# Kernel tuning notes

Hardware: AMD Instinct MI355X
Metric: run time of the kernel (lower is better)

## Reference

```python
import jax, jax.numpy as jnp
import numpy as np

DIM = 192
HEADS = 4
HID = int(DIM * 2.66)  # 510, Restormer GDFN hidden dim
EPS_LN = 1e-6


def ln2d(x, w, b):
    # torch LayerNorm2d variant: global mean/std over (C,H,W), std is UNBIASED (ddof=1)
    n = x.shape[1] * x.shape[2] * x.shape[3]
    mean = x.mean(axis=(1, 2, 3), keepdims=True)
    var = ((x - mean) ** 2).sum(axis=(1, 2, 3), keepdims=True) / (n - 1)
    return (x - mean) / (jnp.sqrt(var) + EPS_LN) * w + b


def conv1x1(x, w):
    # w: [O, C]; pointwise conv as channel matmul
    return jnp.einsum('bchw,oc->bohw', x, w)


def dwconv3(x, w):
    # w: [C, 1, 3, 3] depthwise 3x3, padding=1
    return jax.lax.conv_general_dilated(
        x, w, window_strides=(1, 1), padding='SAME',
        dimension_numbers=('NCHW', 'OIHW', 'NCHW'),
        feature_group_count=x.shape[1])


def setup_inputs() -> dict:
    key = jax.random.key(0)
    ks = jax.random.split(key, 8)
    s = 0.02
    return {
        'x': jax.random.normal(ks[0], (2, DIM, 256, 256), dtype=jnp.float32),
        'n1_w': jnp.ones((1, DIM, 1, 1), jnp.float32),
        'n1_b': jnp.zeros((1, DIM, 1, 1), jnp.float32),
        'qkv_w': jax.random.normal(ks[1], (3 * DIM, DIM), jnp.float32) * s,
        'qkv_dw_w': jax.random.normal(ks[2], (3 * DIM, 1, 3, 3), jnp.float32) * s,
        'proj_w': jax.random.normal(ks[3], (DIM, DIM), jnp.float32) * s,
        'temperature': jnp.ones((HEADS, 1, 1), jnp.float32),
        'n2_w': jnp.ones((1, DIM, 1, 1), jnp.float32),
        'n2_b': jnp.zeros((1, DIM, 1, 1), jnp.float32),
        'ff_in_w': jax.random.normal(ks[4], (2 * HID, DIM), jnp.float32) * s,
        'ff_dw_w': jax.random.normal(ks[5], (2 * HID, 1, 3, 3), jnp.float32) * s,
        'ff_out_w': jax.random.normal(ks[6], (DIM, HID), jnp.float32) * s,
    }


def reference(x, n1_w, n1_b, qkv_w, qkv_dw_w, proj_w, temperature,
              n2_w, n2_b, ff_in_w, ff_dw_w, ff_out_w):
    b, c, h, w = x.shape
    hd = c // HEADS

    # ---- MDTA attention ----
    y = ln2d(x, n1_w, n1_b)
    qkv = dwconv3(conv1x1(y, qkv_w), qkv_dw_w)  # [b, 3c, h, w]
    q, k, v = jnp.split(qkv, 3, axis=1)
    q = q.reshape(b, HEADS, hd, h * w)
    k = k.reshape(b, HEADS, hd, h * w)
    v = v.reshape(b, HEADS, hd, h * w)
    # L2-normalize along spatial axis (F.normalize, eps=1e-12)
    q = q / jnp.maximum(jnp.linalg.norm(q, axis=-1, keepdims=True), 1e-12)
    k = k / jnp.maximum(jnp.linalg.norm(k, axis=-1, keepdims=True), 1e-12)
    attn = jnp.einsum('bhcn,bhdn->bhcd', q, k) * temperature  # [b,H,hd,hd]
    attn = jax.nn.softmax(attn, axis=-1)
    out = jnp.einsum('bhcd,bhdn->bhcn', attn, v).reshape(b, c, h, w)
    x = x + conv1x1(out, proj_w)

    # ---- GDFN feed-forward ----
    y = ln2d(x, n2_w, n2_b)
    y = dwconv3(conv1x1(y, ff_in_w), ff_dw_w)  # [b, 2*HID, h, w]
    x1, x2 = jnp.split(y, 2, axis=1)
    y = jax.nn.gelu(x1, approximate=False) * x2
    x = x + conv1x1(y, ff_out_w)
    return x
```

## Files before the change

### kernel.cpp

```cpp
#include <hip/hip_runtime.h>
#include <hip/hip_bf16.h>

typedef unsigned short u16;
typedef __attribute__((ext_vector_type(8))) short short8;
typedef __attribute__((ext_vector_type(8))) unsigned short ushort8v;
typedef __attribute__((ext_vector_type(4))) float f32x4;

#define NPIX  65536
#define HH    256
#define WW    256
#define BATCH 2
#define CDIM  192
#define NHEADS 4
#define HD    48
#define OQKV  576
#define HIDN  510
#define OPAD  1024

__device__ __forceinline__ float bf2f(u16 b) {
  union { unsigned u; float f; } v; v.u = ((unsigned)b) << 16; return v.f;
}
__device__ __forceinline__ u16 f2bf(float f) {
  union { float f; unsigned u; } v; v.f = f;
  unsigned r = v.u + 0x7fffu + ((v.u >> 16) & 1u);
  return (u16)(r >> 16);
}
__device__ __forceinline__ void atomAddF(float* p, float v) { unsafeAtomicAdd(p, v); }
__device__ __forceinline__ void gload16(const void* g, void* l) {
  __builtin_amdgcn_global_load_lds((const __attribute__((address_space(1))) unsigned int*)g,
                                   (__attribute__((address_space(3))) unsigned int*)l, 16, 0, 0);
}
__device__ __forceinline__ void xcdswz(int& bx, int& by) {
  const int nx = gridDim.x;
  const int tot = nx * gridDim.y;
  const int lin = by * nx + bx;
  const int q = tot >> 3, r = tot & 7;
  const int xcd = lin & 7, pos = lin >> 3;
  const int nl = (xcd < r) ? (xcd * (q + 1) + pos) : (r * (q + 1) + (xcd - r) * q + pos);
  bx = nl % nx; by = nl / nx;
}
__device__ __forceinline__ void dw3row(const u16* __restrict__ rp, int jm, bool hasL, bool hasR,
                                       float w0, float w1, float w2, float* acc) {
  ushort8v m = *(const ushort8v*)(rp + jm);
  float f[10];
  f[0] = hasL ? bf2f(rp[jm - 1]) : 0.f;
  #pragma unroll
  for (int t = 0; t < 8; ++t) f[t + 1] = bf2f(m[t]);
  f[9] = hasR ? bf2f(rp[jm + 8]) : 0.f;
  #pragma unroll
  for (int i = 0; i < 8; ++i) acc[i] += w0 * f[i] + w1 * f[i + 1] + w2 * f[i + 2];
}

#define OFF_STATS1 ((size_t)0)
#define OFF_STATS2 ((size_t)64)
#define OFF_G      ((size_t)128)
#define OFF_NQ     (OFF_G + 73728)
#define OFF_NK     (OFF_NQ + 1536)
#define ZERO_BYTES (OFF_NK + 1536)
#define OFF_BQ     ((size_t)77056)
#define OFF_B2     (OFF_BQ + 4608)
#define OFF_M      (OFF_B2 + 8192)
#define OFF_WQ     (OFF_M + 294912)
#define OFF_W2B    (OFF_WQ + 442368)
#define OFF_W3     (OFF_W2B + 786432)
#define OFF_T      (OFF_W3 + 196608)
#define OFF_QKV    (OFF_T + 50331648)
#define OFF_BAND   (OFF_QKV + 150994944)

__global__ __launch_bounds__(256) void k_statsT(const float* __restrict__ P, u16* __restrict__ T,
                                                float* __restrict__ stats) {
  __shared__ u16 ld[128][200];
  const int b = blockIdx.y, n0 = blockIdx.x * 128, tid = threadIdx.x;
  const float* Pb = P + (((size_t)b * CDIM) << 16) + n0;
  float s = 0.f, ss = 0.f;
  for (int it = 0; it < 24; ++it) {
    int idx = it * 256 + tid;
    int c = idx >> 5, j = idx & 31;
    float4 v = *(const float4*)(Pb + ((size_t)c << 16) + j * 4);
    s  += v.x + v.y + v.z + v.w;
    ss += v.x*v.x + v.y*v.y + v.z*v.z + v.w*v.w;
    int px = j * 4;
    ld[px][c] = f2bf(v.x); ld[px+1][c] = f2bf(v.y);
    ld[px+2][c] = f2bf(v.z); ld[px+3][c] = f2bf(v.w);
  }
  for (int off = 32; off; off >>= 1) { s += __shfl_down(s, off); ss += __shfl_down(ss, off); }
  __shared__ float ls[4], lss[4];
  const int wid = tid >> 6, lane = tid & 63;
  if (lane == 0) { ls[wid] = s; lss[wid] = ss; }
  __syncthreads();
  if (tid == 0) {
    atomAddF(&stats[b*2+0], ls[0]+ls[1]+ls[2]+ls[3]);
    atomAddF(&stats[b*2+1], lss[0]+lss[1]+lss[2]+lss[3]);
  }
  u16* Tb = T + (size_t)(b * NPIX + n0) * CDIM;
  for (int it = 0; it < 12; ++it) {
    int idx = it * 256 + tid;
    int ch = idx % 24, nl = idx / 24;
    union { u16 s[8]; uint4 v; } t;
    #pragma unroll
    for (int r = 0; r < 8; ++r) t.s[r] = ld[nl][ch * 8 + r];
    int sch = ch ^ (nl & 7);
    *(uint4*)((char*)(Tb + (size_t)nl * CDIM) + sch * 16) = t.v;
  }
}

__global__ void k_fold(const float* __restrict__ w_in, const float* __restrict__ ln_w,
                       const float* __restrict__ ln_b, const float* __restrict__ stats,
                       u16* __restrict__ W, float* __restrict__ bias, int O_real) {
  const int o = blockIdx.x, b = blockIdx.y, c = threadIdx.x;
  const int Mtot = gridDim.x;
  const float n = (float)(CDIM * NPIX);
  const float sum = stats[b*2], sumsq = stats[b*2+1];
  const float mean = sum / n;
  const float var = (sumsq - sum * sum / n) / (n - 1.f);
  const float inv = 1.f / (sqrtf(var) + 1e-6f);
  float we = 0.f, cb = 0.f;
  if (o < O_real) {
    float wi = w_in[o * CDIM + c];
    float a  = ln_w[c] * inv;
    we = wi * a;
    cb = wi * (ln_b[c] - mean * a);
  }
  int sch = (c >> 3) ^ (o & 7);
  W[((size_t)b * Mtot + o) * CDIM + sch * 8 + (c & 7)] = f2bf(we);
  for (int off = 32; off; off >>= 1) cb += __shfl_down(cb, off);
  __shared__ float l[3];
  if ((threadIdx.x & 63) == 0) l[threadIdx.x >> 6] = cb;
  __syncthreads();
  if (threadIdx.x == 0) bias[b * Mtot + o] = l[0] + l[1] + l[2];
}

__global__ void k_fold3(const float* __restrict__ w, u16* __restrict__ W3) {
  const int o = blockIdx.x;
  for (int it = 0; it < 2; ++it) {
    int c = it * 256 + threadIdx.x;
    float v = (c < HIDN) ? w[o * HIDN + c] : 0.f;
    int sch = (c >> 3) ^ (o & 7);
    W3[o * 512 + sch * 8 + (c & 7)] = f2bf(v);
  }
}

template <int KTOT, int KC, int EPI, int STATS>
__global__ __launch_bounds__(256) void k_mgemm(
    const u16* __restrict__ Bm, const u16* __restrict__ Am,
    const float* __restrict__ bias,
    const u16* __restrict__ rT, long rTbstr,
    void* __restrict__ outv, long Obstr, int out_nstr,
    u16* __restrict__ tout, long toutbstr,
    int Mtot, long Bbstr, long Abstr,
    int nB_base, int nB_rows, int nO_base, float* __restrict__ stats)
{
  constexpr int RBC = KC * 2;
  __shared__ u16 lB[128 * KC];
  __shared__ u16 lA[64 * KC];
  const int b = blockIdx.z;
  int bx = blockIdx.x, by = blockIdx.y;
  xcdswz(bx, by);
  const int o0 = bx * 64;
  const int nB = nB_base + by * 128;
  const int nO = nO_base + by * 128;
  const int tid = threadIdx.x;
  const int lane = tid & 63;
  const int wid = tid >> 6;

  if (EPI == 0 && (nB < 0 || nB >= nB_rows)) {
    u16* op = (u16*)outv;
    uint4 z; z.x = z.y = z.z = z.w = 0u;
    for (int it = 0; it < 4; ++it) {
      int idx = it * 256 + tid;
      int orow = idx >> 4, c8 = idx & 15;
      *(uint4*)(op + (size_t)b * Obstr + (size_t)(o0 + orow) * out_nstr + nO + c8 * 8) = z;
    }
    return;
  }

  const u16* Bb = Bm + (size_t)b * Bbstr + (size_t)nB * KTOT;
  const u16* Ab = Am + (size_t)b * Abstr + (size_t)o0 * KTOT;

  f32x4 acc[4][2];
  #pragma unroll
  for (int m = 0; m < 4; ++m)
    #pragma unroll
    for (int nf = 0; nf < 2; ++nf) acc[m][nf] = (f32x4){0.f, 0.f, 0.f, 0.f};

  for (int kc0 = 0; kc0 < KTOT; kc0 += KC) {
    if (kc0) __syncthreads();
    if constexpr (KTOT == KC) {
      #pragma unroll
      for (int it = 0; it < 128 * RBC / 16 / 256; ++it) {
        int idx = it * 256 + tid;
        gload16((const char*)Bb + idx * 16, (char*)lB + idx * 16);
      }
      #pragma unroll
      for (int it = 0; it < 64 * RBC / 16 / 256; ++it) {
        int idx = it * 256 + tid;
        gload16((const char*)Ab + idx * 16, (char*)lA + idx * 16);
      }
    } else {
      constexpr int NCH = KC / 8;
      #pragma unroll
      for (int it = 0; it < 128 * NCH / 256; ++it) {
        int idx = it * 256 + tid; int r = idx / NCH, ch = idx % NCH;
        gload16((const char*)(Bb + (size_t)r * KTOT + kc0) + ch * 16, (char*)lB + idx * 16);
      }
      #pragma unroll
      for (int it = 0; it < 64 * NCH / 256; ++it) {
        int idx = it * 256 + tid; int r = idx / NCH, ch = idx % NCH;
        gload16((const char*)(Ab + (size_t)r * KTOT + kc0) + ch * 16, (char*)lA + idx * 16);
      }
    }
    __syncthreads();
    const int lr = lane & 15, g = lane >> 4;
    #pragma unroll
    for (int ks = 0; ks < KC / 32; ++ks) {
      const int ck = ks * 4 + g;
      short8 afr[4], bfr[2];
      #pragma unroll
      for (int m = 0; m < 4; ++m) {
        int row = m * 16 + lr;
        afr[m] = *(const short8*)((const char*)lA + row * RBC + ((ck ^ (row & 7)) << 4));
      }
      #pragma unroll
      for (int nf = 0; nf < 2; ++nf) {
        int row = wid * 32 + nf * 16 + lr;
        bfr[nf] = *(const short8*)((const char*)lB + row * RBC + ((ck ^ (row & 7)) << 4));
      }
      #pragma unroll
      for (int m = 0; m < 4; ++m)
        #pragma unroll
        for (int nf = 0; nf < 2; ++nf)
          acc[m][nf] = __builtin_amdgcn_mfma_f32_16x16x32_bf16(afr[m], bfr[nf], acc[m][nf], 0, 0, 0);
    }
  }

  const int col = lane & 15, rg = lane >> 4;
  if constexpr (EPI == 0) {
    u16* op = (u16*)outv;
    #pragma unroll
    for (int m = 0; m < 4; ++m)
      #pragma unroll
      for (int j = 0; j < 4; ++j) {
        int o = o0 + m * 16 + rg * 4 + j;
        float bv = bias[b * Mtot + o];
        #pragma unroll
        for (int nf = 0; nf < 2; ++nf) {
          int nn = nO + wid * 32 + nf * 16 + col;
          op[(size_t)b * Obstr + (size_t)o * out_nstr + nn] = f2bf(acc[m][nf][j] + bv);
        }
      }
  } else if constexpr (EPI == 2) {
    float* lBf = (float*)lB;
    __syncthreads();
    #pragma unroll
    for (int m = 0; m < 4; ++m)
      #pragma unroll
      for (int nf = 0; nf < 2; ++nf)
        #pragma unroll
        for (int j = 0; j < 4; ++j)
          lBf[(wid * 32 + nf * 16 + col) * 66 + m * 16 + rg * 4 + j] = acc[m][nf][j];
    __syncthreads();
    float s = 0.f, ss = 0.f;
    for (int it = 0; it < 4; ++it) {
      int idx = it * 256 + tid;
      int n = idx >> 3, ch3 = idx & 7;
      size_t rowoff = (size_t)(nO + n) * CDIM;
      int chunk = (o0 >> 3) + (ch3 ^ (n & 7));
      uint4 xv = *(const uint4*)((const char*)(rT + (size_t)b * rTbstr + rowoff) + chunk * 16);
      u16* xs = (u16*)&xv;
      union { u16 s[8]; uint4 v; } t;
      #pragma unroll
      for (int r = 0; r < 8; ++r) {
        float rv = bf2f(xs[r]) + lBf[n * 66 + ch3 * 8 + r];
        t.s[r] = f2bf(rv);
        if constexpr (STATS) { s += rv; ss += rv * rv; }
      }
      *(uint4*)((char*)(tout + (size_t)b * toutbstr + rowoff) + chunk * 16) = t.v;
    }
    if constexpr (STATS) {
      for (int off = 32; off; off >>= 1) { s += __shfl_down(s, off); ss += __shfl_down(ss, off); }
      __shared__ float sr1[4], sr2[4];
      if (lane == 0) { sr1[wid] = s; sr2[wid] = ss; }
      __syncthreads();
      if (tid == 0) {
        atomAddF(&stats[b*2+0], sr1[0]+sr1[1]+sr1[2]+sr1[3]);
        atomAddF(&stats[b*2+1], sr2[0]+sr2[1]+sr2[2]+sr2[3]);
      }
    }
  } else {
    u16* lAx = lA;
    __syncthreads();
    for (int it = 0; it < 4; ++it) {
      int idx = it * 256 + tid;
      int n = idx >> 3, ch3 = idx & 7;
      int chunk = (o0 >> 3) + (ch3 ^ (n & 7));
      uint4 xv = *(const uint4*)((const char*)(rT + (size_t)b * rTbstr + (size_t)(nO + n) * CDIM) + chunk * 16);
      u16* xs = (u16*)&xv;
      #pragma unroll
      for (int r = 0; r < 8; ++r) lAx[n * 66 + ch3 * 8 + r] = xs[r];
    }
    __syncthreads();
    float* of = (float*)outv;
    #pragma unroll
    for (int m = 0; m < 4; ++m)
      #pragma unroll
      for (int nf = 0; nf < 2; ++nf)
        #pragma unroll
        for (int j = 0; j < 4; ++j) {
          int o = o0 + m * 16 + rg * 4 + j;
          int nl = wid * 32 + nf * 16 + col;
          size_t ix = (size_t)b * Obstr + (size_t)o * out_nstr + nO + nl;
          of[ix] = acc[m][nf][j] + bf2f(lAx[nl * 66 + m * 16 + rg * 4 + j]);
        }
  }
}

__global__ __launch_bounds__(256) void k_gram(const u16* __restrict__ qkv,
                                              const float* __restrict__ dww,
                                              float* __restrict__ G,
                                              float* __restrict__ nq,
                                              float* __restrict__ nk) {
  __shared__ u16 qs[HD][264], ks2[HD][264];
  __shared__ u16 wq[HD][9], wk[HD][9];
  __shared__ float nql[HD], nkl[HD];
  int bx = blockIdx.x, by = blockIdx.y;
  xcdswz(bx, by);
  const int b = by >> 2, h = by & 3;
  const int row = bx;
  const int tid = threadIdx.x;

  for (int idx = tid; idx < HD * 9; idx += 256) {
    int c = idx / 9, k9 = idx % 9;
    wq[c][k9] = f2bf(dww[(h * HD + c) * 9 + k9]);
    wk[c][k9] = f2bf(dww[(CDIM + h * HD + c) * 9 + k9]);
  }
  if (tid < HD) { nql[tid] = 0.f; nkl[tid] = 0.f; }
  __syncthreads();

  for (int it = 0; it < 12; ++it) {
    int idx = it * 256 + tid;
    int j = idx & 31, cz = idx >> 5;
    int c = cz % HD, qk = cz / HD;
    const u16* base = qkv + (((size_t)(b * OQKV + qk * CDIM + h * HD + c)) << 16);
    const u16* w = qk ? wk[c] : wq[c];
    float acc[8] = {0.f,0.f,0.f,0.f,0.f,0.f,0.f,0.f};
    const int jm = j * 8;
    const bool hasL = j > 0, hasR = j < 31;
    if (row > 0)   dw3row(base + (row - 1) * 256, jm, hasL, hasR, bf2f(w[0]), bf2f(w[1]), bf2f(w[2]), acc);
                   dw3row(base + row * 256,       jm, hasL, hasR, bf2f(w[3]), bf2f(w[4]), bf2f(w[5]), acc);
    if (row < 255) dw3row(base + (row + 1) * 256, jm, hasL, hasR, bf2f(w[6]), bf2f(w[7]), bf2f(w[8]), acc);
    union { u16 s[8]; ushort8v v; } rv;
    float sqs = 0.f;
    #pragma unroll
    for (int i = 0; i < 8; ++i) {
      rv.s[i] = f2bf(acc[i]);
      float vv = bf2f(rv.s[i]);
      sqs += vv * vv;
    }
    if (qk) { *(ushort8v*)&ks2[c][jm] = rv.v; atomicAdd(&nkl[c], sqs); }
    else    { *(ushort8v*)&qs[c][jm]  = rv.v; atomicAdd(&nql[c], sqs); }
  }
  __syncthreads();

  if (tid < HD) atomAddF(&nq[(b*NHEADS+h)*HD + tid], nql[tid]);
  else if (tid < 2*HD) atomAddF(&nk[(b*NHEADS+h)*HD + tid - HD], nkl[tid - HD]);

  const int lane = tid & 63, wid = tid >> 6;
  const int lr = lane & 15, g = lane >> 4;
  float* Gb = G + (size_t)(b * NHEADS + h) * HD * HD;
  for (int t = wid; t < 9; t += 4) {
    const int m = t / 3, nb = t % 3;
    f32x4 a4 = (f32x4){0.f, 0.f, 0.f, 0.f};
    #pragma unroll
    for (int ksi = 0; ksi < 8; ++ksi) {
      int off = ksi * 32 + g * 8;
      short8 af = *(const short8*)&qs[m * 16 + lr][off];
      short8 bf = *(const short8*)&ks2[nb * 16 + lr][off];
      a4 = __builtin_amdgcn_mfma_f32_16x16x32_bf16(af, bf, a4, 0, 0, 0);
    }
    #pragma unroll
    for (int jj = 0; jj < 4; ++jj)
      atomAddF(&Gb[(m * 16 + g * 4 + jj) * HD + nb * 16 + lr], a4[jj]);
  }
}

__global__ void k_attnM(const float* __restrict__ G, const float* __restrict__ nq,
                        const float* __restrict__ nk, const float* __restrict__ temp,
                        const float* __restrict__ proj_w, u16* __restrict__ Mb16) {
  const int h = blockIdx.x, b = blockIdx.y;
  __shared__ float at[HD][HD];
  const float* Gb = G + (size_t)(b * NHEADS + h) * HD * HD;
  const float* nqb = nq + (b * NHEADS + h) * HD;
  const float* nkb = nk + (b * NHEADS + h) * HD;
  const float t = temp[h];
  const int tid = threadIdx.x;
  for (int idx = tid; idx < HD * HD; idx += 256) {
    int c = idx / HD, d = idx % HD;
    float qn = fmaxf(sqrtf(nqb[c]), 1e-12f);
    float kn = fmaxf(sqrtf(nkb[d]), 1e-12f);
    at[c][d] = Gb[idx] / (qn * kn) * t;
  }
  __syncthreads();
  if (tid < HD) {
    float m = -1e30f;
    for (int d = 0; d < HD; ++d) m = fmaxf(m, at[tid][d]);
    float s = 0.f;
    for (int d = 0; d < HD; ++d) { float e = __expf(at[tid][d] - m); at[tid][d] = e; s += e; }
    float inv = 1.f / s;
    for (int d = 0; d < HD; ++d) at[tid][d] *= inv;
  }
  __syncthreads();
  for (int idx = tid; idx < CDIM * HD; idx += 256) {
    int o = idx / HD, d = idx % HD;
    float acc = 0.f;
    for (int c = 0; c < HD; ++c) acc += proj_w[o * CDIM + h * HD + c] * at[c][d];
    int cf = h * HD + d;
    int sch = (cf >> 3) ^ (o & 7);
    Mb16[((size_t)(b * CDIM + o)) * CDIM + sch * 8 + (cf & 7)] = f2bf(acc);
  }
}

__global__ __launch_bounds__(256) void k_dwT(const u16* __restrict__ qkv,
                                             const float* __restrict__ dww,
                                             u16* __restrict__ vdwT, long vdwbstr) {
  __shared__ u16 ld[64][201];
  __shared__ float w9[CDIM][9];
  int bx = blockIdx.x, by = blockIdx.y;
  xcdswz(bx, by);
  const int b = by;
  const int p0 = bx * 64;
  const int row = p0 >> 8, col0 = p0 & 255;
  const int tid = threadIdx.x;
  for (int idx = tid; idx < CDIM * 9; idx += 256) w9[idx / 9][idx % 9] = dww[384 * 9 + idx];
  __syncthreads();
  for (int it = 0; it < 6; ++it) {
    int idx = it * 256 + tid;
    int j = idx & 7, c = idx >> 3;
    const u16* base = qkv + (((size_t)(b * OQKV + 384 + c)) << 16);
    const float* w = w9[c];
    float acc[8] = {0.f,0.f,0.f,0.f,0.f,0.f,0.f,0.f};
    const int jm = col0 + j * 8;
    const bool hasL = jm > 0, hasR = jm < 248;
    if (row > 0)   dw3row(base + (row - 1) * 256, jm, hasL, hasR, w[0], w[1], w[2], acc);
                   dw3row(base + row * 256,       jm, hasL, hasR, w[3], w[4], w[5], acc);
    if (row < 255) dw3row(base + (row + 1) * 256, jm, hasL, hasR, w[6], w[7], w[8], acc);
    #pragma unroll
    for (int i = 0; i < 8; ++i) ld[j * 8 + i][c] = f2bf(acc[i]);
  }
  __syncthreads();
  u16* Tb = vdwT + (size_t)b * vdwbstr + (size_t)p0 * CDIM;
  for (int it = 0; it < 6; ++it) {
    int idx = it * 256 + tid;
    int ch = idx % 24, pl = idx / 24;
    union { u16 s[8]; uint4 v; } t;
    #pragma unroll
    for (int r = 0; r < 8; ++r) t.s[r] = ld[pl][ch * 8 + r];
    int sch = ch ^ (pl & 7);
    *(uint4*)((char*)(Tb + (size_t)pl * CDIM) + sch * 16) = t.v;
  }
}

__global__ __launch_bounds__(256) void k_dwgT(const u16* __restrict__ hp_, const float* __restrict__ w9,
                                              u16* __restrict__ ygT, int rows_loc, int band_px) {
  __shared__ u16 ld[64][523];
  int bx = blockIdx.x, by = blockIdx.y;
  xcdswz(bx, by);
  const int b = by;
  const int p0 = bx * 64;
  const int olr = p0 >> 8, col0 = p0 & 255;
  const int tid = threadIdx.x;
  if (tid < 128) {
    int px = tid >> 1, c = 510 + (tid & 1);
    ld[px][c] = 0;
  }
  __syncthreads();
  for (int it = 0; it < 16; ++it) {
    int idx = it * 256 + tid;
    if (idx >= HIDN * 8) break;
    int j = idx & 7, c = idx >> 3;
    const u16* ia = hp_ + (size_t)(b * OPAD + c) * rows_loc * 256;
    const u16* ig = hp_ + (size_t)(b * OPAD + c + HIDN) * rows_loc * 256;
    float aa[8] = {0.f,0.f,0.f,0.f,0.f,0.f,0.f,0.f};
    float gg[8] = {0.f,0.f,0.f,0.f,0.f,0.f,0.f,0.f};
    const int jm = col0 + j * 8;
    const bool hasL = jm > 0, hasR = jm < 248;
    #pragma unroll
    for (int dr = 0; dr < 3; ++dr) {
      dw3row(ia + (olr + dr) * 256, jm, hasL, hasR,
             w9[c * 9 + dr * 3], w9[c * 9 + dr * 3 + 1], w9[c * 9 + dr * 3 + 2], aa);
      dw3row(ig + (olr + dr) * 256, jm, hasL, hasR,
             w9[(c + HIDN) * 9 + dr * 3], w9[(c + HIDN) * 9 + dr * 3 + 1],
             w9[(c + HIDN) * 9 + dr * 3 + 2], gg);
    }
    #pragma unroll
    for (int i = 0; i < 8; ++i) {
      float a = aa[i];
      float gel = 0.5f * a * (1.f + erff(a * 0.70710678118654752f));
      ld[j * 8 + i][c] = f2bf(gel * gg[i]);
    }
  }
  __syncthreads();
  u16* Tb = ygT + ((size_t)b * band_px + p0) * 512;
  for (int it = 0; it < 16; ++it) {
    int idx = it * 256 + tid;
    int ch = idx & 63, pl = idx >> 6;
    union { u16 s[8]; uint4 v; } t;
    #pragma unroll
    for (int r = 0; r < 8; ++r) t.s[r] = ld[pl][ch * 8 + r];
    int sch = ch ^ (pl & 7);
    *(uint4*)((char*)(Tb + (size_t)pl * 512) + sch * 16) = t.v;
  }
}

extern "C" void kernel_launch(void* const* d_in, const int* in_sizes, int n_in,
                              void* d_out, int out_size, void* d_ws, size_t ws_size,
                              hipStream_t stream) {
  const float* x       = (const float*)d_in[0];
  const float* n1_w    = (const float*)d_in[1];
  const float* n1_b    = (const float*)d_in[2];
  const float* qkv_w   = (const float*)d_in[3];
  const float* qkv_dw  = (const float*)d_in[4];
  const float* proj_w  = (const float*)d_in[5];
  const float* temp    = (const float*)d_in[6];
  const float* n2_w    = (const float*)d_in[7];
  const float* n2_b    = (const float*)d_in[8];
  const float* ff_in_w = (const float*)d_in[9];
  const float* ff_dw   = (const float*)d_in[10];
  const float* ff_out_w= (const float*)d_in[11];

  char* ws = (char*)d_ws;
  float* stats1 = (float*)(ws + OFF_STATS1);
  float* stats2 = (float*)(ws + OFF_STATS2);
  float* G      = (float*)(ws + OFF_G);
  float* nq     = (float*)(ws + OFF_NQ);
  float* nk     = (float*)(ws + OFF_NK);
  float* biasq  = (float*)(ws + OFF_BQ);
  float* bias2  = (float*)(ws + OFF_B2);
  u16*   Mb16   = (u16*)(ws + OFF_M);
  u16*   Wq     = (u16*)(ws + OFF_WQ);
  u16*   W2b    = (u16*)(ws + OFF_W2B);
  u16*   W3     = (u16*)(ws + OFF_W3);
  u16*   xT     = (u16*)(ws + OFF_T);
  u16*   qkv    = (u16*)(ws + OFF_QKV);
  u16*   vdwT   = qkv;
  u16*   x2T    = qkv + (size_t)CDIM * NPIX;
  const long qkvbstr = (long)OQKV * NPIX;
  float* outp   = (float*)d_out;

  int NP = 32;
  const int cand[4] = {2, 4, 8, 16};
  for (int i = 0; i < 4; ++i) {
    int rws = 256 / cand[i], rl = rws + 2;
    size_t band = (size_t)2 * OPAD * rl * 256 * 2 + (size_t)2 * rws * 256 * 512 * 2;
    if (OFF_BAND + band + ((size_t)8 << 20) <= ws_size) { NP = cand[i]; break; }
  }
  const int rows = 256 / NP, rows_loc = rows + 2, band_px = rows * 256;
  u16* hpre = (u16*)(ws + OFF_BAND);
  u16* ygT  = (u16*)(ws + OFF_BAND + (size_t)2 * OPAD * rows_loc * 256 * 2);

  hipMemsetAsync(ws, 0, ZERO_BYTES, stream);

  k_statsT<<<dim3(NPIX / 128, BATCH), 256, 0, stream>>>(x, xT, stats1);
  k_fold<<<dim3(OQKV, BATCH), CDIM, 0, stream>>>(qkv_w, n1_w, n1_b, stats1, Wq, biasq, OQKV);
  k_mgemm<192, 192, 0, 0><<<dim3(OQKV / 64, NPIX / 128, BATCH), 256, 0, stream>>>(
      xT, Wq, biasq, nullptr, 0L, qkv, (long)OQKV * NPIX, NPIX, nullptr, 0L,
      OQKV, (long)NPIX * CDIM, (long)OQKV * CDIM, 0, NPIX, 0, nullptr);
  k_gram<<<dim3(256, BATCH * NHEADS), 256, 0, stream>>>(qkv, qkv_dw, G, nq, nk);
  k_attnM<<<dim3(NHEADS, BATCH), 256, 0, stream>>>(G, nq, nk, temp, proj_w, Mb16);
  k_dwT<<<dim3(NPIX / 64, BATCH), 256, 0, stream>>>(qkv, qkv_dw, vdwT, qkvbstr);
  k_mgemm<192, 192, 2, 1><<<dim3(CDIM / 64, NPIX / 128, BATCH), 256, 0, stream>>>(
      vdwT, Mb16, nullptr, xT, (long)NPIX * CDIM, nullptr, 0L, 0, x2T, qkvbstr,
      CDIM, qkvbstr, (long)CDIM * CDIM, 0, NPIX, 0, stats2);

  k_fold<<<dim3(OPAD, BATCH), CDIM, 0, stream>>>(ff_in_w, n2_w, n2_b, stats2, W2b, bias2, 1020);
  k_fold3<<<dim3(CDIM), 256, 0, stream>>>(ff_out_w, W3);
  for (int rp = 0; rp < NP; ++rp) {
    const int band0 = rp * band_px;
    k_mgemm<192, 192, 0, 0><<<dim3(OPAD / 64, rows_loc * 2, BATCH), 256, 0, stream>>>(
        x2T, W2b, bias2, nullptr, 0L, hpre, (long)OPAD * rows_loc * 256, rows_loc * 256,
        nullptr, 0L, OPAD, qkvbstr, (long)OPAD * CDIM, band0 - 256, NPIX, 0, nullptr);
    k_dwgT<<<dim3(band_px / 64, BATCH), 256, 0, stream>>>(hpre, ff_dw, ygT, rows_loc, band_px);
    k_mgemm<512, 256, 3, 0><<<dim3(CDIM / 64, rows * 2, BATCH), 256, 0, stream>>>(
        ygT, W3, nullptr, x2T, qkvbstr, outp, (long)CDIM * NPIX, NPIX, nullptr, 0L,
        CDIM, (long)band_px * 512, 0L, 0, band_px, band0, nullptr);
  }
}
```

Baseline: 892.7 us.

## Spread reduction atomics over slots and shrink GEMM K-chunks for occupancy

Global atomic accumulators for LayerNorm statistics, the Gram matrix and the q/k norms are spread over 32 slots, so blocks stop contending on the same addresses. The consumers (fold, attnM) sum the slots when they read them. The GEMM kernels now use smaller K chunks (64 or 128 instead of 192 or 256) in a single union LDS buffer that the epilogue reuses, which cuts shared memory per block and should allow more resident blocks. The cost is extra K-loop iterations with more barriers, and a larger zeroed workspace. The swizzle must stay correct when K is chunked.

Result: faster. 807.7 us (-9.5%).

```diff
diff --git a/kernel.cpp b/kernel.cpp
--- a/kernel.cpp
+++ b/kernel.cpp
@@ -16,6 +16,7 @@
 #define OQKV  576
 #define HIDN  510
 #define OPAD  1024
+#define NSLOT 32
 
 __device__ __forceinline__ float bf2f(u16 b) {
   union { unsigned u; float f; } v; v.u = ((unsigned)b) << 16; return v.f;
@@ -52,12 +53,12 @@
 }
 
 #define OFF_STATS1 ((size_t)0)
-#define OFF_STATS2 ((size_t)64)
-#define OFF_G      ((size_t)128)
-#define OFF_NQ     (OFF_G + 73728)
-#define OFF_NK     (OFF_NQ + 1536)
-#define ZERO_BYTES (OFF_NK + 1536)
-#define OFF_BQ     ((size_t)77056)
+#define OFF_STATS2 ((size_t)512)
+#define OFF_G      ((size_t)1024)
+#define OFF_NQ     (OFF_G + 2359296)
+#define OFF_NK     (OFF_NQ + 49152)
+#define ZERO_BYTES (OFF_NK + 49152)
+#define OFF_BQ     ZERO_BYTES
 #define OFF_B2     (OFF_BQ + 4608)
 #define OFF_M      (OFF_B2 + 8192)
 #define OFF_WQ     (OFF_M + 294912)
@@ -71,6 +72,7 @@
                                                 float* __restrict__ stats) {
   __shared__ u16 ld[128][200];
   const int b = blockIdx.y, n0 = blockIdx.x * 128, tid = threadIdx.x;
+  const int slot = blockIdx.x & (NSLOT - 1);
   const float* Pb = P + (((size_t)b * CDIM) << 16) + n0;
   float s = 0.f, ss = 0.f;
   for (int it = 0; it < 24; ++it) {
@@ -89,8 +91,8 @@
   if (lane == 0) { ls[wid] = s; lss[wid] = ss; }
   __syncthreads();
   if (tid == 0) {
-    atomAddF(&stats[b*2+0], ls[0]+ls[1]+ls[2]+ls[3]);
-    atomAddF(&stats[b*2+1], lss[0]+lss[1]+lss[2]+lss[3]);
+    atomAddF(&stats[(slot * BATCH + b) * 2 + 0], ls[0]+ls[1]+ls[2]+ls[3]);
+    atomAddF(&stats[(slot * BATCH + b) * 2 + 1], lss[0]+lss[1]+lss[2]+lss[3]);
   }
   u16* Tb = T + (size_t)(b * NPIX + n0) * CDIM;
   for (int it = 0; it < 12; ++it) {
@@ -110,7 +112,11 @@
   const int o = blockIdx.x, b = blockIdx.y, c = threadIdx.x;
   const int Mtot = gridDim.x;
   const float n = (float)(CDIM * NPIX);
-  const float sum = stats[b*2], sumsq = stats[b*2+1];
+  float sum = 0.f, sumsq = 0.f;
+  for (int sl = 0; sl < NSLOT; ++sl) {
+    sum   += stats[(sl * BATCH + b) * 2 + 0];
+    sumsq += stats[(sl * BATCH + b) * 2 + 1];
+  }
   const float mean = sum / n;
   const float var = (sumsq - sum * sum / n) / (n - 1.f);
   const float inv = 1.f / (sqrtf(var) + 1e-6f);
@@ -151,8 +157,12 @@
     int nB_base, int nB_rows, int nO_base, float* __restrict__ stats)
 {
   constexpr int RBC = KC * 2;
-  __shared__ u16 lB[128 * KC];
-  __shared__ u16 lA[64 * KC];
+  constexpr int LDSB = (128 + 64) * KC * 2;
+  constexpr int EPIB = (EPI == 2) ? 128 * 66 * 4 : ((EPI == 3) ? 128 * 66 * 2 : 0);
+  constexpr int TOT  = LDSB > EPIB ? LDSB : EPIB;
+  __shared__ char lds[TOT];
+  u16* lB = (u16*)lds;
+  u16* lA = (u16*)(lds + 128 * KC * 2);
   const int b = blockIdx.z;
   int bx = blockIdx.x, by = blockIdx.y;
   xcdswz(bx, by);
@@ -185,29 +195,16 @@
 
   for (int kc0 = 0; kc0 < KTOT; kc0 += KC) {
     if (kc0) __syncthreads();
-    if constexpr (KTOT == KC) {
-      #pragma unroll
-      for (int it = 0; it < 128 * RBC / 16 / 256; ++it) {
-        int idx = it * 256 + tid;
-        gload16((const char*)Bb + idx * 16, (char*)lB + idx * 16);
-      }
-      #pragma unroll
-      for (int it = 0; it < 64 * RBC / 16 / 256; ++it) {
-        int idx = it * 256 + tid;
-        gload16((const char*)Ab + idx * 16, (char*)lA + idx * 16);
-      }
-    } else {
-      constexpr int NCH = KC / 8;
-      #pragma unroll
-      for (int it = 0; it < 128 * NCH / 256; ++it) {
-        int idx = it * 256 + tid; int r = idx / NCH, ch = idx % NCH;
-        gload16((const char*)(Bb + (size_t)r * KTOT + kc0) + ch * 16, (char*)lB + idx * 16);
-      }
-      #pragma unroll
-      for (int it = 0; it < 64 * NCH / 256; ++it) {
-        int idx = it * 256 + tid; int r = idx / NCH, ch = idx % NCH;
-        gload16((const char*)(Ab + (size_t)r * KTOT + kc0) + ch * 16, (char*)lA + idx * 16);
-      }
+    constexpr int NCH = KC / 8;
+    #pragma unroll
+    for (int it = 0; it < 128 * NCH / 256; ++it) {
+      int idx = it * 256 + tid; int r = idx / NCH, ch = idx % NCH;
+      gload16((const char*)(Bb + (size_t)r * KTOT + kc0) + ch * 16, (char*)lB + idx * 16);
+    }
+    #pragma unroll
+    for (int it = 0; it < 64 * NCH / 256; ++it) {
+      int idx = it * 256 + tid; int r = idx / NCH, ch = idx % NCH;
+      gload16((const char*)(Ab + (size_t)r * KTOT + kc0) + ch * 16, (char*)lA + idx * 16);
     }
     __syncthreads();
     const int lr = lane & 15, g = lane >> 4;
@@ -249,7 +246,7 @@
         }
       }
   } else if constexpr (EPI == 2) {
-    float* lBf = (float*)lB;
+    float* lBf = (float*)lds;
     __syncthreads();
     #pragma unroll
     for (int m = 0; m < 4; ++m)
@@ -282,12 +279,13 @@
       if (lane == 0) { sr1[wid] = s; sr2[wid] = ss; }
       __syncthreads();
       if (tid == 0) {
-        atomAddF(&stats[b*2+0], sr1[0]+sr1[1]+sr1[2]+sr1[3]);
-        atomAddF(&stats[b*2+1], sr2[0]+sr2[1]+sr2[2]+sr2[3]);
+        int slot = by & (NSLOT - 1);
+        atomAddF(&stats[(slot * BATCH + b) * 2 + 0], sr1[0]+sr1[1]+sr1[2]+sr1[3]);
+        atomAddF(&stats[(slot * BATCH + b) * 2 + 1], sr2[0]+sr2[1]+sr2[2]+sr2[3]);
       }
     }
   } else {
-    u16* lAx = lA;
+    u16* lAx = (u16*)lds;
     __syncthreads();
     for (int it = 0; it < 4; ++it) {
       int idx = it * 256 + tid;
@@ -326,6 +324,8 @@
   xcdswz(bx, by);
   const int b = by >> 2, h = by & 3;
   const int row = bx;
+  const int slot = row & (NSLOT - 1);
+  const int bh = b * NHEADS + h;
   const int tid = threadIdx.x;
 
   for (int idx = tid; idx < HD * 9; idx += 256) {
@@ -361,12 +361,12 @@
   }
   __syncthreads();
 
-  if (tid < HD) atomAddF(&nq[(b*NHEADS+h)*HD + tid], nql[tid]);
-  else if (tid < 2*HD) atomAddF(&nk[(b*NHEADS+h)*HD + tid - HD], nkl[tid - HD]);
+  if (tid < HD) atomAddF(&nq[(slot * 2 * NHEADS + bh) * HD + tid], nql[tid]);
+  else if (tid < 2*HD) atomAddF(&nk[(slot * 2 * NHEADS + bh) * HD + tid - HD], nkl[tid - HD]);
 
   const int lane = tid & 63, wid = tid >> 6;
   const int lr = lane & 15, g = lane >> 4;
-  float* Gb = G + (size_t)(b * NHEADS + h) * HD * HD;
+  float* Gb = G + (size_t)(slot * 2 * NHEADS + bh) * HD * HD;
   for (int t = wid; t < 9; t += 4) {
     const int m = t / 3, nb = t % 3;
     f32x4 a4 = (f32x4){0.f, 0.f, 0.f, 0.f};
@@ -387,17 +387,28 @@
                         const float* __restrict__ nk, const float* __restrict__ temp,
                         const float* __restrict__ proj_w, u16* __restrict__ Mb16) {
   const int h = blockIdx.x, b = blockIdx.y;
+  const int bh = b * NHEADS + h;
   __shared__ float at[HD][HD];
-  const float* Gb = G + (size_t)(b * NHEADS + h) * HD * HD;
-  const float* nqb = nq + (b * NHEADS + h) * HD;
-  const float* nkb = nk + (b * NHEADS + h) * HD;
+  __shared__ float nqs[HD], nks[HD];
+  const int tid = threadIdx.x;
+  if (tid < HD) {
+    float s = 0.f;
+    for (int sl = 0; sl < NSLOT; ++sl) s += nq[(sl * 2 * NHEADS + bh) * HD + tid];
+    nqs[tid] = fmaxf(sqrtf(s), 1e-12f);
+  } else if (tid >= 64 && tid < 64 + HD) {
+    int c = tid - 64;
+    float s = 0.f;
+    for (int sl = 0; sl < NSLOT; ++sl) s += nk[(sl * 2 * NHEADS + bh) * HD + c];
+    nks[c] = fmaxf(sqrtf(s), 1e-12f);
+  }
+  __syncthreads();
   const float t = temp[h];
-  const int tid = threadIdx.x;
   for (int idx = tid; idx < HD * HD; idx += 256) {
     int c = idx / HD, d = idx % HD;
-    float qn = fmaxf(sqrtf(nqb[c]), 1e-12f);
-    float kn = fmaxf(sqrtf(nkb[d]), 1e-12f);
-    at[c][d] = Gb[idx] / (qn * kn) * t;
+    float g = 0.f;
+    for (int sl = 0; sl < NSLOT; ++sl)
+      g += G[(size_t)(sl * 2 * NHEADS + bh) * HD * HD + idx];
+    at[c][d] = g / (nqs[c] * nks[d]) * t;
   }
   __syncthreads();
   if (tid < HD) {
@@ -561,13 +572,13 @@
 
   k_statsT<<<dim3(NPIX / 128, BATCH), 256, 0, stream>>>(x, xT, stats1);
   k_fold<<<dim3(OQKV, BATCH), CDIM, 0, stream>>>(qkv_w, n1_w, n1_b, stats1, Wq, biasq, OQKV);
-  k_mgemm<192, 192, 0, 0><<<dim3(OQKV / 64, NPIX / 128, BATCH), 256, 0, stream>>>(
+  k_mgemm<192, 64, 0, 0><<<dim3(OQKV / 64, NPIX / 128, BATCH), 256, 0, stream>>>(
       xT, Wq, biasq, nullptr, 0L, qkv, (long)OQKV * NPIX, NPIX, nullptr, 0L,
       OQKV, (long)NPIX * CDIM, (long)OQKV * CDIM, 0, NPIX, 0, nullptr);
   k_gram<<<dim3(256, BATCH * NHEADS), 256, 0, stream>>>(qkv, qkv_dw, G, nq, nk);
   k_attnM<<<dim3(NHEADS, BATCH), 256, 0, stream>>>(G, nq, nk, temp, proj_w, Mb16);
   k_dwT<<<dim3(NPIX / 64, BATCH), 256, 0, stream>>>(qkv, qkv_dw, vdwT, qkvbstr);
-  k_mgemm<192, 192, 2, 1><<<dim3(CDIM / 64, NPIX / 128, BATCH), 256, 0, stream>>>(
+  k_mgemm<192, 64, 2, 1><<<dim3(CDIM / 64, NPIX / 128, BATCH), 256, 0, stream>>>(
       vdwT, Mb16, nullptr, xT, (long)NPIX * CDIM, nullptr, 0L, 0, x2T, qkvbstr,
       CDIM, qkvbstr, (long)CDIM * CDIM, 0, NPIX, 0, stats2);
 
@@ -575,11 +586,11 @@
   k_fold3<<<dim3(CDIM), 256, 0, stream>>>(ff_out_w, W3);
   for (int rp = 0; rp < NP; ++rp) {
     const int band0 = rp * band_px;
-    k_mgemm<192, 192, 0, 0><<<dim3(OPAD / 64, rows_loc * 2, BATCH), 256, 0, stream>>>(
+    k_mgemm<192, 64, 0, 0><<<dim3(OPAD / 64, rows_loc * 2, BATCH), 256, 0, stream>>>(
         x2T, W2b, bias2, nullptr, 0L, hpre, (long)OPAD * rows_loc * 256, rows_loc * 256,
         nullptr, 0L, OPAD, qkvbstr, (long)OPAD * CDIM, band0 - 256, NPIX, 0, nullptr);
     k_dwgT<<<dim3(band_px / 64, BATCH), 256, 0, stream>>>(hpre, ff_dw, ygT, rows_loc, band_px);
-    k_mgemm<512, 256, 3, 0><<<dim3(CDIM / 64, rows * 2, BATCH), 256, 0, stream>>>(
+    k_mgemm<512, 128, 3, 0><<<dim3(CDIM / 64, rows * 2, BATCH), 256, 0, stream>>>(
         ygT, W3, nullptr, x2T, qkvbstr, outp, (long)CDIM * NPIX, NPIX, nullptr, 0L,
         CDIM, (long)band_px * 512, 0L, 0, band_px, band0, nullptr);
   }
```
